# Optimization experiments

Hardware: AMD Instinct MI355X
Metric: run time of the kernel (lower is better)

The kernel has to match this reference:

```python
import jax, jax.numpy as jnp
import numpy as np

N_NODES = 50000
N_EDGES = 800000
IN_DIM = 128
HEADS = 8
HEAD_DIM = 16
NEG_SLOPE = 0.2  # DGL GATConv default LeakyReLU slope
BN_EPS = 1e-5


def setup_inputs() -> dict:
    key = jax.random.key(0)
    ks = jax.random.split(key, 8)
    h = jax.random.normal(ks[0], (N_NODES, IN_DIM), dtype=jnp.float32)
    src = jax.random.randint(ks[1], (N_EDGES,), 0, N_NODES, dtype=jnp.int64)
    dst = jax.random.randint(ks[2], (N_EDGES,), 0, N_NODES, dtype=jnp.int64)
    W = jax.random.normal(ks[3], (IN_DIM, HEADS * HEAD_DIM), dtype=jnp.float32) * 0.1
    attn_l = jax.random.normal(ks[4], (HEADS, HEAD_DIM), dtype=jnp.float32) * 0.1
    attn_r = jax.random.normal(ks[5], (HEADS, HEAD_DIM), dtype=jnp.float32) * 0.1
    gamma = jnp.ones((HEADS * HEAD_DIM,), dtype=jnp.float32)
    beta = jnp.zeros((HEADS * HEAD_DIM,), dtype=jnp.float32)
    return {"h": h, "src": src, "dst": dst, "W": W, "attn_l": attn_l,
            "attn_r": attn_r, "gamma": gamma, "beta": beta}


def reference(h, src, dst, W, attn_l, attn_r, gamma, beta):
    N = h.shape[0]
    H, D = attn_l.shape
    # linear projection (no bias, matching DGL GATConv fc)
    feat = (h @ W).reshape(N, H, D)                       # [N,H,D]
    el = jnp.sum(feat * attn_l, axis=-1)                  # [N,H]
    er = jnp.sum(feat * attn_r, axis=-1)                  # [N,H]
    # per-edge attention logits: LeakyReLU(el[src] + er[dst])
    e = jax.nn.leaky_relu(el[src] + er[dst], NEG_SLOPE)   # [E,H]
    # edge softmax over incoming edges of each destination node
    emax = jax.ops.segment_max(e, dst, num_segments=N)    # [N,H]
    ee = jnp.exp(e - emax[dst])                           # [E,H]
    denom = jax.ops.segment_sum(ee, dst, num_segments=N)  # [N,H]
    alpha = ee / denom[dst]                               # [E,H]
    # weighted scatter-aggregate of source features
    msg = alpha[:, :, None] * feat[src]                   # [E,H,D]
    out = jax.ops.segment_sum(msg, dst, num_segments=N)   # [N,H,D]
    out = out.reshape(N, H * D)                           # flatten(1)
    # BatchNorm1d (training-mode batch statistics)
    mean = out.mean(axis=0)
    var = out.var(axis=0)
    out = gamma * (out - mean) * jax.lax.rsqrt(var + BN_EPS) + beta
    # ELU activation then residual
    out = jax.nn.elu(out)
    return h + out
```

## Files before the change

### kernel.cpp

```cpp
#include <hip/hip_runtime.h>
#include <math.h>

#define N_NODES 50000
#define N_EDGES 800000
#define NEG_SLOPE 0.2f
#define BN_EPS 1e-5f

#define CAP 96

#define WS_FEAT    0u
#define WS_EL      25600000u
#define WS_ER      27200000u
#define WS_CURSOR  28800000u
#define WS_GPART   29000704u
#define WS_CSR     29008896u
#define ZERO_START WS_CURSOR
#define ZERO_BYTES (WS_CSR - WS_CURSOR)

#define GEMM_TILES 782
#define SCAT_BLOCKS 3125
#define AGG_BLOCKS 1024
#define AGG_WAVES (AGG_BLOCKS * 4)

__global__ __launch_bounds__(256) void k1(
    const float* __restrict__ hin, const float* __restrict__ W,
    const float* __restrict__ attn_l, const float* __restrict__ attn_r,
    const int* __restrict__ src, const int* __restrict__ dst,
    int* __restrict__ cursor, int* __restrict__ csr,
    float* __restrict__ feat, float* __restrict__ el, float* __restrict__ er)
{
    __shared__ float Hs[64 * 132];

    if (blockIdx.x >= GEMM_TILES) {
        int i = (blockIdx.x - GEMM_TILES) * 256 + threadIdx.x;
        if (i < N_EDGES) {
            int s = src[i], d = dst[i];
            int slot = atomicAdd(&cursor[d], 1);
            if (slot < CAP) csr[d * CAP + slot] = s;
        }
        return;
    }

    const int t = threadIdx.x;
    const int row0 = blockIdx.x * 64;

    const float4* h4 = (const float4*)hin;
    #pragma unroll
    for (int i = 0; i < 8; i++) {
        int idx = t + 256 * i;
        int r = idx >> 5, c4 = idx & 31;
        int gr = row0 + r;
        float4 v = make_float4(0.f, 0.f, 0.f, 0.f);
        if (gr < N_NODES) v = h4[gr * 32 + c4];
        *(float4*)&Hs[r * 132 + c4 * 4] = v;
    }
    __syncthreads();

    const int tx = t & 15, ty = t >> 4;
    const int c0 = tx * 8, r0 = ty * 4;

    float acc[4][8];
    #pragma unroll
    for (int r = 0; r < 4; r++)
        #pragma unroll
        for (int j = 0; j < 8; j++) acc[r][j] = 0.f;

    const float4* W4 = (const float4*)W;
    const float4* A0 = (const float4*)&Hs[(r0 + 0) * 132];
    const float4* A1 = (const float4*)&Hs[(r0 + 1) * 132];
    const float4* A2 = (const float4*)&Hs[(r0 + 2) * 132];
    const float4* A3 = (const float4*)&Hs[(r0 + 3) * 132];

    #pragma unroll 2
    for (int k4 = 0; k4 < 32; k4++) {
        float4 a0 = A0[k4], a1 = A1[k4], a2 = A2[k4], a3 = A3[k4];
        float Av0[4] = {a0.x, a0.y, a0.z, a0.w};
        float Av1[4] = {a1.x, a1.y, a1.z, a1.w};
        float Av2[4] = {a2.x, a2.y, a2.z, a2.w};
        float Av3[4] = {a3.x, a3.y, a3.z, a3.w};
        int kb = k4 * 4;
        #pragma unroll
        for (int kk = 0; kk < 4; kk++) {
            float4 b0 = W4[(kb + kk) * 32 + tx * 2];
            float4 b1 = W4[(kb + kk) * 32 + tx * 2 + 1];
            float av[4] = {Av0[kk], Av1[kk], Av2[kk], Av3[kk]};
            #pragma unroll
            for (int r = 0; r < 4; r++) {
                acc[r][0] += av[r] * b0.x; acc[r][1] += av[r] * b0.y;
                acc[r][2] += av[r] * b0.z; acc[r][3] += av[r] * b0.w;
                acc[r][4] += av[r] * b1.x; acc[r][5] += av[r] * b1.y;
                acc[r][6] += av[r] * b1.z; acc[r][7] += av[r] * b1.w;
            }
        }
    }

    const int h = tx >> 1;
    const int dbase = (tx & 1) * 8;
    float elv[4], erv[4];
    #pragma unroll
    for (int r = 0; r < 4; r++) {
        float e = 0.f, f = 0.f;
        #pragma unroll
        for (int j = 0; j < 8; j++) {
            float al = attn_l[h * 16 + dbase + j];
            float ar = attn_r[h * 16 + dbase + j];
            e += acc[r][j] * al; f += acc[r][j] * ar;
        }
        elv[r] = e + __shfl_xor(e, 1);
        erv[r] = f + __shfl_xor(f, 1);
    }

    #pragma unroll
    for (int r = 0; r < 4; r++) {
        int gr = row0 + r0 + r;
        if (gr < N_NODES) {
            *(float4*)&feat[gr * 128 + c0] =
                make_float4(acc[r][0], acc[r][1], acc[r][2], acc[r][3]);
            *(float4*)&feat[gr * 128 + c0 + 4] =
                make_float4(acc[r][4], acc[r][5], acc[r][6], acc[r][7]);
            if ((tx & 1) == 0) { el[gr * 8 + h] = elv[r]; er[gr * 8 + h] = erv[r]; }
        }
    }
}

__global__ __launch_bounds__(256) void k_agg(
    const float* __restrict__ feat, const float* __restrict__ el,
    const float* __restrict__ er, const int* __restrict__ cursor,
    const int* __restrict__ csr, float* __restrict__ outf,
    float* __restrict__ gpart)
{
    __shared__ float rs[512], rq[512];
    int t = threadIdx.x, lane = t & 63, w = t >> 6;
    int h = lane >> 3;
    const float2* feat2 = (const float2*)feat;

    float bs0 = 0.f, bq0 = 0.f, bs1 = 0.f, bq1 = 0.f;

    for (int n = (blockIdx.x * 256 + t) >> 6; n < N_NODES; n += AGG_WAVES) {
        int cnt = cursor[n]; if (cnt > CAP) cnt = CAP;
        const int* bucket = csr + n * CAP;
        float er_nh = er[n * 8 + h];
        float sum = 0.f, ax = 0.f, ay = 0.f;
        int p = 0;
        for (; p + 4 <= cnt; p += 4) {
            int s0 = bucket[p + 0], s1 = bucket[p + 1];
            int s2 = bucket[p + 2], s3 = bucket[p + 3];
            float e0 = el[s0 * 8 + h] + er_nh;
            float e1 = el[s1 * 8 + h] + er_nh;
            float e2 = el[s2 * 8 + h] + er_nh;
            float e3 = el[s3 * 8 + h] + er_nh;
            e0 = e0 > 0.f ? e0 : NEG_SLOPE * e0;
            e1 = e1 > 0.f ? e1 : NEG_SLOPE * e1;
            e2 = e2 > 0.f ? e2 : NEG_SLOPE * e2;
            e3 = e3 > 0.f ? e3 : NEG_SLOPE * e3;
            float a0 = __expf(e0), a1 = __expf(e1);
            float a2 = __expf(e2), a3 = __expf(e3);
            float2 f0 = feat2[s0 * 64 + lane];
            float2 f1 = feat2[s1 * 64 + lane];
            float2 f2 = feat2[s2 * 64 + lane];
            float2 f3 = feat2[s3 * 64 + lane];
            sum += (a0 + a1) + (a2 + a3);
            ax += a0 * f0.x; ay += a0 * f0.y;
            ax += a1 * f1.x; ay += a1 * f1.y;
            ax += a2 * f2.x; ay += a2 * f2.y;
            ax += a3 * f3.x; ay += a3 * f3.y;
        }
        for (; p < cnt; p++) {
            int s = bucket[p];
            float e = el[s * 8 + h] + er_nh;
            e = e > 0.f ? e : NEG_SLOPE * e;
            float a = __expf(e);
            float2 f = feat2[s * 64 + lane];
            sum += a; ax += a * f.x; ay += a * f.y;
        }
        float rden = sum > 0.f ? 1.f / sum : 0.f;
        float ox = ax * rden, oy = ay * rden;
        ((float2*)outf)[n * 64 + lane] = make_float2(ox, oy);
        bs0 += ox; bq0 += ox * ox; bs1 += oy; bq1 += oy * oy;
    }

    rs[w * 128 + lane * 2]     = bs0;
    rs[w * 128 + lane * 2 + 1] = bs1;
    rq[w * 128 + lane * 2]     = bq0;
    rq[w * 128 + lane * 2 + 1] = bq1;
    __syncthreads();
    float* gp = gpart + (blockIdx.x & 7) * 256;
    if (t < 128) {
        float s = rs[t] + rs[128 + t] + rs[256 + t] + rs[384 + t];
        atomicAdd(&gp[t], s);
    } else {
        int c = t - 128;
        float q = rq[c] + rq[128 + c] + rq[256 + c] + rq[384 + c];
        atomicAdd(&gp[128 + c], q);
    }
}

__global__ __launch_bounds__(256) void k_final(
    const float* __restrict__ hin, const float* __restrict__ gpart,
    const float* __restrict__ gamma, const float* __restrict__ beta,
    float* __restrict__ out)
{
    int i = blockIdx.x * blockDim.x + threadIdx.x;
    if (i >= N_NODES * 32) return;
    int c4 = i & 31;

    float4 sm = make_float4(0.f, 0.f, 0.f, 0.f);
    float4 sq = make_float4(0.f, 0.f, 0.f, 0.f);
    #pragma unroll
    for (int r = 0; r < 8; r++) {
        float4 a = ((const float4*)(gpart + r * 256))[c4];
        float4 b = ((const float4*)(gpart + r * 256 + 128))[c4];
        sm.x += a.x; sm.y += a.y; sm.z += a.z; sm.w += a.w;
        sq.x += b.x; sq.y += b.y; sq.z += b.z; sq.w += b.w;
    }

    float4 x  = ((const float4*)out)[i];
    float4 hv = ((const float4*)hin)[i];
    float4 g  = ((const float4*)gamma)[c4];
    float4 bt = ((const float4*)beta)[c4];
    const float invN = 1.0f / (float)N_NODES;

    float mean, var, rstd, y;
    mean = sm.x * invN; var = sq.x * invN - mean * mean; rstd = rsqrtf(var + BN_EPS);
    y = g.x * (x.x - mean) * rstd + bt.x; y = y > 0.f ? y : (__expf(y) - 1.f); x.x = hv.x + y;
    mean = sm.y * invN; var = sq.y * invN - mean * mean; rstd = rsqrtf(var + BN_EPS);
    y = g.y * (x.y - mean) * rstd + bt.y; y = y > 0.f ? y : (__expf(y) - 1.f); x.y = hv.y + y;
    mean = sm.z * invN; var = sq.z * invN - mean * mean; rstd = rsqrtf(var + BN_EPS);
    y = g.z * (x.z - mean) * rstd + bt.z; y = y > 0.f ? y : (__expf(y) - 1.f); x.z = hv.z + y;
    mean = sm.w * invN; var = sq.w * invN - mean * mean; rstd = rsqrtf(var + BN_EPS);
    y = g.w * (x.w - mean) * rstd + bt.w; y = y > 0.f ? y : (__expf(y) - 1.f); x.w = hv.w + y;

    ((float4*)out)[i] = x;
}

extern "C" void kernel_launch(void* const* d_in, const int* in_sizes, int n_in,
                              void* d_out, int out_size, void* d_ws, size_t ws_size,
                              hipStream_t stream)
{
    const float* hin    = (const float*)d_in[0];
    const int*   src    = (const int*)d_in[1];
    const int*   dst    = (const int*)d_in[2];
    const float* W      = (const float*)d_in[3];
    const float* attn_l = (const float*)d_in[4];
    const float* attn_r = (const float*)d_in[5];
    const float* gamma  = (const float*)d_in[6];
    const float* beta   = (const float*)d_in[7];
    float* out = (float*)d_out;

    char* ws = (char*)d_ws;
    float* feat   = (float*)(ws + WS_FEAT);
    float* el     = (float*)(ws + WS_EL);
    float* er     = (float*)(ws + WS_ER);
    int*   cursor = (int*)(ws + WS_CURSOR);
    float* gpart  = (float*)(ws + WS_GPART);
    int*   csr    = (int*)(ws + WS_CSR);

    hipMemsetAsync(ws + ZERO_START, 0, ZERO_BYTES, stream);
    k1<<<GEMM_TILES + SCAT_BLOCKS, 256, 0, stream>>>(
        hin, W, attn_l, attn_r, src, dst, cursor, csr, feat, el, er);
    k_agg<<<AGG_BLOCKS, 256, 0, stream>>>(feat, el, er, cursor, csr, out, gpart);
    k_final<<<(N_NODES * 32) / 256, 256, 0, stream>>>(hin, gpart, gamma, beta, out);
}
```

Measured before the change: 229.2 us.

## Store projected features in fp16 and widen aggregation grid and stat partitions

The projected node features are written as half precision instead of float, which halves the bytes gathered per edge in the aggregation kernel; values are converted back to float before accumulation. The aggregation grid is doubled and the BatchNorm partial-sum buffer is split into 16 slots instead of 8 to reduce atomic contention. The workspace offset for the CSR buffer is moved to fit the larger partial buffer. Feature precision drops to fp16, which adds rounding error to the output.

```diff
diff --git a/kernel.cpp b/kernel.cpp
--- a/kernel.cpp
+++ b/kernel.cpp
@@ -1,4 +1,5 @@
 #include <hip/hip_runtime.h>
+#include <hip/hip_fp16.h>
 #include <math.h>
 
 #define N_NODES 50000
@@ -13,21 +14,22 @@
 #define WS_ER      27200000u
 #define WS_CURSOR  28800000u
 #define WS_GPART   29000704u
-#define WS_CSR     29008896u
+#define WS_CSR     29017088u
 #define ZERO_START WS_CURSOR
 #define ZERO_BYTES (WS_CSR - WS_CURSOR)
 
 #define GEMM_TILES 782
 #define SCAT_BLOCKS 3125
-#define AGG_BLOCKS 1024
+#define AGG_BLOCKS 2048
 #define AGG_WAVES (AGG_BLOCKS * 4)
+#define NPART 16
 
 __global__ __launch_bounds__(256) void k1(
     const float* __restrict__ hin, const float* __restrict__ W,
     const float* __restrict__ attn_l, const float* __restrict__ attn_r,
     const int* __restrict__ src, const int* __restrict__ dst,
     int* __restrict__ cursor, int* __restrict__ csr,
-    float* __restrict__ feat, float* __restrict__ el, float* __restrict__ er)
+    __half* __restrict__ feath, float* __restrict__ el, float* __restrict__ er)
 {
     __shared__ float Hs[64 * 132];
 
@@ -114,17 +116,23 @@
     for (int r = 0; r < 4; r++) {
         int gr = row0 + r0 + r;
         if (gr < N_NODES) {
-            *(float4*)&feat[gr * 128 + c0] =
-                make_float4(acc[r][0], acc[r][1], acc[r][2], acc[r][3]);
-            *(float4*)&feat[gr * 128 + c0 + 4] =
-                make_float4(acc[r][4], acc[r][5], acc[r][6], acc[r][7]);
+            __half2 p0 = __floats2half2_rn(acc[r][0], acc[r][1]);
+            __half2 p1 = __floats2half2_rn(acc[r][2], acc[r][3]);
+            __half2 p2 = __floats2half2_rn(acc[r][4], acc[r][5]);
+            __half2 p3 = __floats2half2_rn(acc[r][6], acc[r][7]);
+            uint4 u;
+            u.x = *(unsigned int*)&p0;
+            u.y = *(unsigned int*)&p1;
+            u.z = *(unsigned int*)&p2;
+            u.w = *(unsigned int*)&p3;
+            *(uint4*)&feath[gr * 128 + c0] = u;
             if ((tx & 1) == 0) { el[gr * 8 + h] = elv[r]; er[gr * 8 + h] = erv[r]; }
         }
     }
 }
 
 __global__ __launch_bounds__(256) void k_agg(
-    const float* __restrict__ feat, const float* __restrict__ el,
+    const __half* __restrict__ feath, const float* __restrict__ el,
     const float* __restrict__ er, const int* __restrict__ cursor,
     const int* __restrict__ csr, float* __restrict__ outf,
     float* __restrict__ gpart)
@@ -132,7 +140,7 @@
     __shared__ float rs[512], rq[512];
     int t = threadIdx.x, lane = t & 63, w = t >> 6;
     int h = lane >> 3;
-    const float2* feat2 = (const float2*)feat;
+    const __half2* feat2 = (const __half2*)feath;
 
     float bs0 = 0.f, bq0 = 0.f, bs1 = 0.f, bq1 = 0.f;
 
@@ -155,10 +163,10 @@
             e3 = e3 > 0.f ? e3 : NEG_SLOPE * e3;
             float a0 = __expf(e0), a1 = __expf(e1);
             float a2 = __expf(e2), a3 = __expf(e3);
-            float2 f0 = feat2[s0 * 64 + lane];
-            float2 f1 = feat2[s1 * 64 + lane];
-            float2 f2 = feat2[s2 * 64 + lane];
-            float2 f3 = feat2[s3 * 64 + lane];
+            float2 f0 = __half22float2(feat2[s0 * 64 + lane]);
+            float2 f1 = __half22float2(feat2[s1 * 64 + lane]);
+            float2 f2 = __half22float2(feat2[s2 * 64 + lane]);
+            float2 f3 = __half22float2(feat2[s3 * 64 + lane]);
             sum += (a0 + a1) + (a2 + a3);
             ax += a0 * f0.x; ay += a0 * f0.y;
             ax += a1 * f1.x; ay += a1 * f1.y;
@@ -170,7 +178,7 @@
             float e = el[s * 8 + h] + er_nh;
             e = e > 0.f ? e : NEG_SLOPE * e;
             float a = __expf(e);
-            float2 f = feat2[s * 64 + lane];
+            float2 f = __half22float2(feat2[s * 64 + lane]);
             sum += a; ax += a * f.x; ay += a * f.y;
         }
         float rden = sum > 0.f ? 1.f / sum : 0.f;
@@ -184,7 +192,7 @@
     rq[w * 128 + lane * 2]     = bq0;
     rq[w * 128 + lane * 2 + 1] = bq1;
     __syncthreads();
-    float* gp = gpart + (blockIdx.x & 7) * 256;
+    float* gp = gpart + (blockIdx.x & (NPART - 1)) * 256;
     if (t < 128) {
         float s = rs[t] + rs[128 + t] + rs[256 + t] + rs[384 + t];
         atomicAdd(&gp[t], s);
@@ -207,7 +215,7 @@
     float4 sm = make_float4(0.f, 0.f, 0.f, 0.f);
     float4 sq = make_float4(0.f, 0.f, 0.f, 0.f);
     #pragma unroll
-    for (int r = 0; r < 8; r++) {
+    for (int r = 0; r < NPART; r++) {
         float4 a = ((const float4*)(gpart + r * 256))[c4];
         float4 b = ((const float4*)(gpart + r * 256 + 128))[c4];
         sm.x += a.x; sm.y += a.y; sm.z += a.z; sm.w += a.w;
@@ -248,7 +256,7 @@
     float* out = (float*)d_out;
 
     char* ws = (char*)d_ws;
-    float* feat   = (float*)(ws + WS_FEAT);
+    __half* feath = (__half*)(ws + WS_FEAT);
     float* el     = (float*)(ws + WS_EL);
     float* er     = (float*)(ws + WS_ER);
     int*   cursor = (int*)(ws + WS_CURSOR);
@@ -257,7 +265,7 @@
 
     hipMemsetAsync(ws + ZERO_START, 0, ZERO_BYTES, stream);
     k1<<<GEMM_TILES + SCAT_BLOCKS, 256, 0, stream>>>(
-        hin, W, attn_l, attn_r, src, dst, cursor, csr, feat, el, er);
-    k_agg<<<AGG_BLOCKS, 256, 0, stream>>>(feat, el, er, cursor, csr, out, gpart);
+        hin, W, attn_l, attn_r, src, dst, cursor, csr, feath, el, er);
+    k_agg<<<AGG_BLOCKS, 256, 0, stream>>>(feath, el, er, cursor, csr, out, gpart);
     k_final<<<(N_NODES * 32) / 256, 256, 0, stream>>>(hin, gpart, gamma, beta, out);
 }
```

After: 209.7 us. 8.5% less time.
